# Kernel optimization log

Measured on AMD Instinct MI355X. Metric: run time of the kernel, lower is better.

Reference implementation:

```python
import jax, jax.numpy as jnp
import numpy as np

LN_EPS = 1e-5


def lstm_cell(x, h, c, Wih, Whh, b):
    # PyTorch gate order: i, f, g, o
    gates = x @ Wih.T + h @ Whh.T + b
    i, f, g, o = jnp.split(gates, 4, axis=-1)
    c = jax.nn.sigmoid(f) * c + jax.nn.sigmoid(i) * jnp.tanh(g)
    h = jax.nn.sigmoid(o) * jnp.tanh(c)
    return h, c


def run_lstm_layer(xs, Wih, Whh, b, reverse=False):
    # xs: (T, B, D) -> ys: (T, B, H); zero initial state, matching nn.LSTM default
    B = xs.shape[1]
    H = Whh.shape[1]
    init = (jnp.zeros((B, H), xs.dtype), jnp.zeros((B, H), xs.dtype))

    def step(carry, x):
        h, c = lstm_cell(x, carry[0], carry[1], Wih, Whh, b)
        return (h, c), h

    _, ys = jax.lax.scan(step, init, xs, reverse=reverse)
    return ys


def forward(x, enc0_Wih, enc0_Whh, enc0_b, enc1_Wih, enc1_Whh, enc1_b,
            fc_z_W, fc_z_b, ln_g, ln_b, fc_init_W, fc_init_b,
            dec0_Wih, dec0_Whh, dec0_b, dec1_Wih, dec1_Whh, dec1_b,
            fc_out_W, fc_out_b):
    B, T, In = x.shape
    H = dec0_Whh.shape[1]
    L = 2  # num_layers

    # ---------- Encoder: 2-layer bidirectional LSTM ----------
    xs = jnp.transpose(x, (1, 0, 2))  # (T, B, In)
    # layer 0 (index 0 = forward dir, 1 = backward dir)
    f0 = run_lstm_layer(xs, enc0_Wih[0], enc0_Whh[0], enc0_b[0], reverse=False)
    b0 = run_lstm_layer(xs, enc0_Wih[1], enc0_Whh[1], enc0_b[1], reverse=True)
    h0cat = jnp.concatenate([f0, b0], axis=-1)  # (T, B, 2H); inter-layer dropout = identity (eval)
    # layer 1
    f1 = run_lstm_layer(h0cat, enc1_Wih[0], enc1_Whh[0], enc1_b[0], reverse=False)
    b1 = run_lstm_layer(h0cat, enc1_Wih[1], enc1_Whh[1], enc1_b[1], reverse=True)
    last_out = jnp.concatenate([f1[-1], b1[-1]], axis=-1)  # (B, 2H) == out[:, -1, :]

    zz = last_out @ fc_z_W.T + fc_z_b  # dropout = identity in eval
    mu = jnp.mean(zz, axis=-1, keepdims=True)
    var = jnp.mean((zz - mu) ** 2, axis=-1, keepdims=True)
    z = (zz - mu) * jax.lax.rsqrt(var + LN_EPS) * ln_g + ln_b  # (B, latent)

    # torch: fc_init(z).view(num_layers, batch, hidden) -- raw row-major reshape
    h_init = (z @ fc_init_W.T + fc_init_b).reshape(L, B, H)
    c_init = jnp.zeros_like(h_init)

    inp0 = jnp.zeros((B, In), x.dtype)

    def dec_step(carry, _):
        inp, h0, c0, h1, c1 = carry
        h0, c0 = lstm_cell(inp, h0, c0, dec0_Wih, dec0_Whh, dec0_b)
        h1, c1 = lstm_cell(h0, h1, c1, dec1_Wih, dec1_Whh, dec1_b)
        pred = h1 @ fc_out_W.T + fc_out_b  # dropout = identity (eval)
        # teacher_forcing_ratio = 0.0 path: feed back detached prediction
        return (jax.lax.stop_gradient(pred), h0, c0, h1, c1), pred

    carry0 = (inp0, h_init[0], c_init[0], h_init[1], c_init[1])
    _, preds = jax.lax.scan(dec_step, carry0, None, length=T)  # (T, B, In)
    x_hat = jnp.transpose(preds, (1, 0, 2))  # (B, T, In)
    return x_hat, z


def setup_inputs() -> dict:
    key = jax.random.key(0)
    B, T, In, H, Lat = 2048, 100, 64, 128, 32
    ks = iter(jax.random.split(key, 32))
    s = 0.08  # weight scale for stability
    d = {
        'x': jax.random.normal(next(ks), (B, T, In), jnp.float32),
        'enc0_Wih': s * jax.random.normal(next(ks), (2, 4 * H, In), jnp.float32),
        'enc0_Whh': s * jax.random.normal(next(ks), (2, 4 * H, H), jnp.float32),
        'enc0_b': s * jax.random.normal(next(ks), (2, 4 * H), jnp.float32),
        'enc1_Wih': s * jax.random.normal(next(ks), (2, 4 * H, 2 * H), jnp.float32),
        'enc1_Whh': s * jax.random.normal(next(ks), (2, 4 * H, H), jnp.float32),
        'enc1_b': s * jax.random.normal(next(ks), (2, 4 * H), jnp.float32),
        'fc_z_W': s * jax.random.normal(next(ks), (Lat, 2 * H), jnp.float32),
        'fc_z_b': s * jax.random.normal(next(ks), (Lat,), jnp.float32),
        'ln_g': jnp.ones((Lat,), jnp.float32),
        'ln_b': jnp.zeros((Lat,), jnp.float32),
        'fc_init_W': s * jax.random.normal(next(ks), (2 * H, Lat), jnp.float32),
        'fc_init_b': s * jax.random.normal(next(ks), (2 * H,), jnp.float32),
        'dec0_Wih': s * jax.random.normal(next(ks), (4 * H, In), jnp.float32),
        'dec0_Whh': s * jax.random.normal(next(ks), (4 * H, H), jnp.float32),
        'dec0_b': s * jax.random.normal(next(ks), (4 * H,), jnp.float32),
        'dec1_Wih': s * jax.random.normal(next(ks), (4 * H, H), jnp.float32),
        'dec1_Whh': s * jax.random.normal(next(ks), (4 * H, H), jnp.float32),
        'dec1_b': s * jax.random.normal(next(ks), (4 * H,), jnp.float32),
        'fc_out_W': s * jax.random.normal(next(ks), (In, H), jnp.float32),
        'fc_out_b': s * jax.random.normal(next(ks), (In,), jnp.float32),
    }
    return d


def reference(x, enc0_Wih, enc0_Whh, enc0_b, enc1_Wih, enc1_Whh, enc1_b,
              fc_z_W, fc_z_b, ln_g, ln_b, fc_init_W, fc_init_b,
              dec0_Wih, dec0_Whh, dec0_b, dec1_Wih, dec1_Whh, dec1_b,
              fc_out_W, fc_out_b):
    return forward(x, enc0_Wih, enc0_Whh, enc0_b, enc1_Wih, enc1_Whh, enc1_b,
                   fc_z_W, fc_z_b, ln_g, ln_b, fc_init_W, fc_init_b,
                   dec0_Wih, dec0_Whh, dec0_b, dec1_Wih, dec1_Whh, dec1_b,
                   fc_out_W, fc_out_b)
```

## Files before the change

kernel.cpp:

```cpp
#include <hip/hip_runtime.h>

using u32 = unsigned int;
using u16 = unsigned short;

typedef __attribute__((ext_vector_type(8))) short bfrag;
typedef __attribute__((ext_vector_type(4))) float f32x4;

constexpr int T_ = 100, B_ = 2048;
constexpr size_t X_HAT_SZ = (size_t)B_ * T_ * 64;

constexpr size_t PKB    = 26214400;
constexpr size_t PK_A0  = PKB + 0;
constexpr size_t PK_A1  = PKB + 32768;
constexpr size_t PK_A2  = PKB + 65536;
constexpr size_t PK_A3  = PKB + 131072;
constexpr size_t PK_A4  = PKB + 196608;
constexpr size_t PK_A5  = PKB + 327680;
constexpr size_t PK_A6  = PKB + 458752;
constexpr size_t PK_A7  = PKB + 524288;
constexpr size_t PK_A8  = PKB + 557056;
constexpr size_t PK_A9  = PKB + 622592;
constexpr size_t PK_A10 = PKB + 688128;
constexpr size_t PK_A11 = PKB + 753664;
constexpr size_t PK_ENDU = PKB + 761856;
constexpr size_t O_FCZT  = PK_ENDU * 2;
constexpr size_t O_FCIT  = O_FCZT + 32768;
constexpr size_t O_FINIT = O_FCIT + 32768;

__device__ __forceinline__ u16 f2bfu(float f) {
  u32 u = __float_as_uint(f);
  u += 0x7fffu + ((u >> 16) & 1u);
  return (u16)(u >> 16);
}
__device__ __forceinline__ float bf2f(u32 s) { return __uint_as_float(s << 16); }

__device__ __forceinline__ float sigf(float v) {
  return __builtin_amdgcn_rcpf(1.f + __expf(-v));
}
__device__ __forceinline__ float tanhfast(float v) {
  float a = fabsf(v);
  float e = __expf(-2.f * a);
  float t = fmaf(-2.f * e, __builtin_amdgcn_rcpf(1.f + e), 1.f);
  return v < 0.f ? -t : t;
}

template <int N>
__device__ __forceinline__ void pinA(bfrag* W) {
#pragma unroll
  for (int i = 0; i < N; ++i) asm volatile("" : "+a"(W[i]));
}

__device__ __forceinline__ bfrag ldA(const u16* buf, int strideHalf, int kt, int lane) {
  return *(const bfrag*)(buf + (lane & 15) * strideHalf + kt * 32 + (lane >> 4) * 8);
}

template <int NKT>
__device__ __forceinline__ void mm(f32x4 acc[4], const bfrag* A, const u16* WP, int w, int lane) {
#pragma unroll
  for (int kt = 0; kt < NKT; ++kt) {
#pragma unroll
    for (int g = 0; g < 4; ++g) {
      bfrag bw = *(const bfrag*)(WP + (((size_t)(kt * 32 + g * 8 + w)) * 64 + lane) * 8);
      acc[g] = __builtin_amdgcn_mfma_f32_16x16x32_bf16(A[kt], bw, acc[g], 0, 0, 0);
    }
  }
}

template <int NKT>
__device__ __forceinline__ void loadW(bfrag* W, const u16* wsu, size_t base, int w, int lane) {
#pragma unroll
  for (int kt = 0; kt < NKT; ++kt)
#pragma unroll
    for (int g = 0; g < 4; ++g)
      W[kt * 4 + g] = *(const bfrag*)(wsu + base + (((size_t)(kt * 32 + g * 8 + w)) * 64 + lane) * 8);
}

template <int NKT>
__device__ __forceinline__ void mmR(f32x4 acc[4], const u16* lds, int sh, const bfrag* W, int lane) {
#pragma unroll
  for (int kt = 0; kt < NKT; ++kt) {
    bfrag a = ldA(lds, sh, kt, lane);
#pragma unroll
    for (int g = 0; g < 4; ++g)
      acc[g] = __builtin_amdgcn_mfma_f32_16x16x32_bf16(a, W[kt * 4 + g], acc[g], 0, 0, 0);
  }
}

template <int NKT>
__device__ __forceinline__ void mmL(f32x4 acc[4], const u16* alds, int sh,
                                    const u16* wlds, int w, int lane) {
#pragma unroll
  for (int kt = 0; kt < NKT; ++kt) {
    bfrag a = ldA(alds, sh, kt, lane);
#pragma unroll
    for (int g = 0; g < 4; ++g) {
      bfrag b = *(const bfrag*)(wlds + ((size_t)(kt * 32 + g * 8 + w) * 64 + lane) * 8);
      acc[g] = __builtin_amdgcn_mfma_f32_16x16x32_bf16(a, b, acc[g], 0, 0, 0);
    }
  }
}

__device__ __forceinline__ void cellfin(const f32x4 acc[4], float c[4], u16 hq[4]) {
#pragma unroll
  for (int q = 0; q < 4; ++q) {
    float iv = sigf(acc[0][q]);
    float fv = sigf(acc[1][q]);
    float gv = tanhfast(acc[2][q]);
    float ov = sigf(acc[3][q]);
    c[q] = fmaf(fv, c[q], iv * gv);
    hq[q] = f2bfu(ov * tanhfast(c[q]));
  }
}

__global__ void pack_kernel(const float* e0wih, const float* e0whh,
                            const float* e1wih, const float* e1whh,
                            const float* d0wih, const float* d0whh,
                            const float* d1wih, const float* d1whh,
                            const float* fczw, const float* fciw, const float* fcow,
                            char* ws) {
  int idx = blockIdx.x * 256 + threadIdx.x;
  u16* wsu = (u16*)ws;

  const float* srcs[12] = { e0wih, e0wih + 512 * 64, e0whh, e0whh + 512 * 128,
                            e1wih, e1wih + 512 * 256, e1whh,
                            d0wih, d0whh, d1wih, d1whh, fcow };
  const int Ks[12]  = { 64, 64, 128, 128, 256, 256, 128, 64, 128, 128, 128, 128 };
  const int NFs[12] = { 32, 32, 32, 32, 32, 32, 32, 32, 32, 32, 32, 4 };
  const int cnt[12] = { 32768, 32768, 65536, 65536, 131072, 131072, 65536,
                        32768, 65536, 65536, 65536, 8192 };
  const size_t dst[12] = { PK_A0, PK_A1, PK_A2, PK_A3, PK_A4, PK_A5, PK_A6,
                           PK_A7, PK_A8, PK_A9, PK_A10, PK_A11 };
#pragma unroll
  for (int p = 0; p < 12; ++p) {
    if (idx < cnt[p]) {
      int NF = NFs[p], K = Ks[p];
      int kt = idx / (NF * 512);
      int rem = idx - kt * NF * 512;
      int nf = rem >> 9;
      int li = rem & 511;
      int lane = li >> 3, j = li & 7;
      int n = nf * 16 + (lane & 15);
      int k = kt * 32 + (lane >> 4) * 8 + j;
      wsu[dst[p] + idx] = f2bfu(srcs[p][(size_t)n * K + k]);
      return;
    }
    idx -= cnt[p];
  }
  if (idx < 8192) {
    int k = idx >> 5, l = idx & 31;
    ((float*)(ws + O_FCZT))[idx] = fczw[(size_t)l * 256 + k];
    return;
  }
  idx -= 8192;
  if (idx < 8192) {
    int l = idx >> 8, o = idx & 255;
    ((float*)(ws + O_FCIT))[idx] = fciw[(size_t)o * 32 + l];
    return;
  }
}
constexpr int PACK_TOTAL = 761856 + 16384;
constexpr int PACK_GRID = (PACK_TOTAL + 255) / 256;

__global__ __attribute__((amdgpu_flat_work_group_size(512, 512), amdgpu_waves_per_eu(2, 2)))
void enc01_kernel(
    const float* __restrict__ x, const float* __restrict__ e0b,
    char* __restrict__ ws, float* __restrict__ out) {
  __shared__ __align__(16) u16 xbuf[2][16 * 72];
  __shared__ __align__(16) u16 hbuf[2][16 * 136];

  const int tid = threadIdx.x;
  const int lane = tid & 63, w = tid >> 6;
  const int mode = blockIdx.x >> 7;
  const int chunk = blockIdx.x & 127;
  const int b0r = chunk * 16;
  const u16* wsu = (const u16*)ws;
  const int uu = 16 * w + (lane & 15);
  const int rg = lane >> 4;
  const bool rev = (mode == 0);
  u16* dst = rev ? (u16*)out : (u16*)ws;

  bfrag Wi[8], Wh[16];
  loadW<2>(Wi, wsu, rev ? PK_A1 : PK_A0, w, lane);
  loadW<4>(Wh, wsu, rev ? PK_A3 : PK_A2, w, lane);
  pinA<8>(Wi);
  pinA<16>(Wh);
  const float* bias = e0b + (rev ? 512 : 0);
  const float bi = bias[uu], bf = bias[128 + uu], bg = bias[256 + uu], bo = bias[384 + uu];

  const int xr = tid >> 5, xcp = (tid & 31) * 2;
  auto ldx = [&](int t) {
    return *(const float2*)(x + ((size_t)(b0r + xr) * T_ + t) * 64 + xcp);
  };

  for (int i = tid; i < 2 * 16 * 136; i += 512) (&hbuf[0][0])[i] = 0;
  float c[4] = {0.f, 0.f, 0.f, 0.f};
  float2 pf = ldx(rev ? T_ - 1 : 0);
  *(u32*)&xbuf[0][xr * 72 + xcp] = ((u32)f2bfu(pf.y) << 16) | f2bfu(pf.x);
  __syncthreads();
  pf = ldx(rev ? T_ - 2 : 1);

  int p = 0;
  for (int s = 0; s < T_; ++s) {
    int t = rev ? T_ - 1 - s : s;
    f32x4 acc[4] = { {bi,bi,bi,bi}, {bf,bf,bf,bf}, {bg,bg,bg,bg}, {bo,bo,bo,bo} };
    mmR<2>(acc, xbuf[p], 72, Wi, lane);
    mmR<4>(acc, hbuf[p], 136, Wh, lane);
    u16 hq[4];
    cellfin(acc, c, hq);
#pragma unroll
    for (int q = 0; q < 4; ++q) {
      int row = rg * 4 + q;
      hbuf[1 - p][row * 136 + uu] = hq[q];
      dst[(((size_t)chunk * T_ + t) * 16 + row) * 128 + uu] = hq[q];
    }
    if (s < T_ - 1)
      *(u32*)&xbuf[1 - p][xr * 72 + xcp] = ((u32)f2bfu(pf.y) << 16) | f2bfu(pf.x);
    if (s < T_ - 2) pf = ldx(rev ? t - 2 : t + 2);
    __syncthreads();
    p ^= 1;
  }
}

constexpr int E2_A6   = 0;
constexpr int E2_CAT  = 131072;
constexpr int E2_HB   = 147968;
constexpr int E2_LAST = 0;
constexpr int E2_ZB   = 16384;

__global__ __attribute__((amdgpu_flat_work_group_size(512, 512), amdgpu_waves_per_eu(2, 2)))
void enc2_kernel(
    const float* __restrict__ e1b, const float* __restrict__ fczb,
    const float* __restrict__ lng, const float* __restrict__ lnb,
    const float* __restrict__ fcib,
    char* __restrict__ ws, float* __restrict__ out) {
  __shared__ __align__(16) char sm[156672];
  u16* A6L = (u16*)(sm + E2_A6);

  const int tid = threadIdx.x;
  const int lane = tid & 63, w = tid >> 6;
  const int chunk = blockIdx.x;
  const int b0r = chunk * 16;
  const u16* wsu = (const u16*)ws;
  const int uu = 16 * w + (lane & 15);
  const int rg = lane >> 4;

  {
    const uint4* src = (const uint4*)(wsu + PK_A6);
    uint4* d = (uint4*)A6L;
    for (int i = tid; i < 8192; i += 512) d[i] = src[i];
  }
  bfrag W4[32];
  loadW<8>(W4, wsu, PK_A4, w, lane);
  pinA<32>(W4);
  const float bi = e1b[uu], bf = e1b[128 + uu], bg = e1b[256 + uu], bo = e1b[384 + uu];
  {
    u16* hb0 = (u16*)(sm + E2_HB);
    for (int i = tid; i < 2 * 16 * 136; i += 512) hb0[i] = 0;
  }
  float c[4] = {0.f, 0.f, 0.f, 0.f};

  const u32* f0u = (const u32*)ws;
  const u32* b0u = (const u32*)out;
  const int prow = tid >> 6, pc4 = tid & 63;
  auto ldrow = [&](const u32* src, int t, int r) {
    return src[(((size_t)chunk * T_ + t) * 16 + r) * 64 + pc4];
  };
  u32 pa = ldrow(f0u, 0, prow), pb = ldrow(f0u, 0, prow + 8);
  u32 pc = ldrow(b0u, 0, prow), pd = ldrow(b0u, 0, prow + 8);
  {
    u16* cat0 = (u16*)(sm + E2_CAT);
    *(u32*)&cat0[prow * 264 + pc4 * 2] = pa;
    *(u32*)&cat0[(prow + 8) * 264 + pc4 * 2] = pb;
    *(u32*)&cat0[prow * 264 + 128 + pc4 * 2] = pc;
    *(u32*)&cat0[(prow + 8) * 264 + 128 + pc4 * 2] = pd;
  }
  __syncthreads();
  pa = ldrow(f0u, 1, prow); pb = ldrow(f0u, 1, prow + 8);
  pc = ldrow(b0u, 1, prow); pd = ldrow(b0u, 1, prow + 8);

  int p = 0;
  for (int t = 0; t < T_; ++t) {
    u16* catP = (u16*)(sm + E2_CAT + p * 8448);
    u16* catN = (u16*)(sm + E2_CAT + (1 - p) * 8448);
    u16* hbP  = (u16*)(sm + E2_HB + p * 4352);
    u16* hbN  = (u16*)(sm + E2_HB + (1 - p) * 4352);
    f32x4 acc[4] = { {bi,bi,bi,bi}, {bf,bf,bf,bf}, {bg,bg,bg,bg}, {bo,bo,bo,bo} };
    mmR<8>(acc, catP, 264, W4, lane);
    mmL<4>(acc, hbP, 136, A6L, w, lane);
    if (t < T_ - 1) {
      *(u32*)&catN[prow * 264 + pc4 * 2] = pa;
      *(u32*)&catN[(prow + 8) * 264 + pc4 * 2] = pb;
      *(u32*)&catN[prow * 264 + 128 + pc4 * 2] = pc;
      *(u32*)&catN[(prow + 8) * 264 + 128 + pc4 * 2] = pd;
    }
    if (t < T_ - 2) {
      pa = ldrow(f0u, t + 2, prow); pb = ldrow(f0u, t + 2, prow + 8);
      pc = ldrow(b0u, t + 2, prow); pd = ldrow(b0u, t + 2, prow + 8);
    }
    u16 hq[4];
    cellfin(acc, c, hq);
#pragma unroll
    for (int q = 0; q < 4; ++q) hbN[(rg * 4 + q) * 136 + uu] = hq[q];
    __syncthreads();
    p ^= 1;
  }

  float* lastout = (float*)(sm + E2_LAST);
  float* zbuf = (float*)(sm + E2_ZB);
  {
    u16* cat99 = (u16*)(sm + E2_CAT + 8448);
    u16* hb99  = (u16*)(sm + E2_HB);
    const float* b = e1b + 512;
    float bi2 = b[uu], bf2 = b[128 + uu], bg2 = b[256 + uu], bo2 = b[384 + uu];
    bfrag a8[8];
#pragma unroll
    for (int kt = 0; kt < 8; ++kt) a8[kt] = ldA(cat99, 264, kt, lane);
    f32x4 acc[4] = { {bi2,bi2,bi2,bi2}, {bf2,bf2,bf2,bf2}, {bg2,bg2,bg2,bg2}, {bo2,bo2,bo2,bo2} };
    mm<8>(acc, a8, wsu + PK_A5, w, lane);
    __syncthreads();
#pragma unroll
    for (int q = 0; q < 4; ++q) {
      float iv = sigf(acc[0][q]);
      float gv = tanhfast(acc[2][q]);
      float ov = sigf(acc[3][q]);
      float cv = iv * gv;
      lastout[(rg * 4 + q) * 256 + 128 + uu] = ov * tanhfast(cv);
    }
    for (int i = tid; i < 2048; i += 512) {
      int r = i >> 7, cc = i & 127;
      lastout[r * 256 + cc] = bf2f(hb99[r * 136 + cc]);
    }
    __syncthreads();
  }

  {
    int r = tid >> 5, l = tid & 31;
    const float* fczT = (const float*)(ws + O_FCZT);
    float acc = fczb[l];
    for (int k = 0; k < 256; ++k) acc = fmaf(lastout[r * 256 + k], fczT[k * 32 + l], acc);
    float s1 = acc, s2 = acc * acc;
#pragma unroll
    for (int off = 16; off >= 1; off >>= 1) {
      s1 += __shfl_xor(s1, off, 32);
      s2 += __shfl_xor(s2, off, 32);
    }
    float mu = s1 * (1.f / 32.f);
    float var = s2 * (1.f / 32.f) - mu * mu;
    float zv = (acc - mu) * rsqrtf(var + 1e-5f) * lng[l] + lnb[l];
    zbuf[r * 32 + l] = zv;
    out[X_HAT_SZ + (size_t)(b0r + r) * 32 + l] = zv;
  }
  __syncthreads();

  {
    const float* fciT = (const float*)(ws + O_FCIT);
    float* finit = (float*)(ws + O_FINIT);
    int o = tid & 255, half = tid >> 8;
#pragma unroll
    for (int rr = 0; rr < 8; ++rr) {
      int r = half * 8 + rr;
      float acc = fcib[o];
#pragma unroll
      for (int l = 0; l < 32; ++l) acc = fmaf(zbuf[r * 32 + l], fciT[l * 256 + o], acc);
      finit[(size_t)(b0r + r) * 256 + o] = acc;
    }
  }
}

constexpr int DC_A10 = 0;
constexpr int DC_XB  = 131072;
constexpr int DC_HA  = 135680;
constexpr int DC_HB  = 144384;
__global__ __attribute__((amdgpu_flat_work_group_size(512, 512), amdgpu_waves_per_eu(2, 2)))
void dec_kernel(
    const float* __restrict__ d0b, const float* __restrict__ d1b,
    const float* __restrict__ fcob,
    char* __restrict__ ws, float* __restrict__ out) {
  __shared__ __align__(16) char sm[153088];
  u16* A10L = (u16*)(sm + DC_A10);

  const int tid = threadIdx.x;
  const int lane = tid & 63, w = tid >> 6;
  const int chunk = blockIdx.x;
  const int b0r = chunk * 16;
  const u16* wsu = (const u16*)ws;
  const float* finit = (const float*)(ws + O_FINIT);
  const int uu = 16 * w + (lane & 15);
  const int rg = lane >> 4;

  {
    const uint4* src = (const uint4*)(wsu + PK_A10);
    uint4* d = (uint4*)A10L;
    for (int i = tid; i < 8192; i += 512) d[i] = src[i];
  }
  bfrag W7[8], W8[16], W9[16], W11[4];
  loadW<2>(W7, wsu, PK_A7, w, lane);
  loadW<4>(W8, wsu, PK_A8, w, lane);
  loadW<4>(W9, wsu, PK_A9, w, lane);
  {
    int wf = w & 3;
#pragma unroll
    for (int kt = 0; kt < 4; ++kt)
      W11[kt] = *(const bfrag*)(wsu + PK_A11 + (((size_t)(kt * 4 + wf)) * 64 + lane) * 8);
  }
  pinA<8>(W7);
  pinA<16>(W8);
  pinA<16>(W9);
  pinA<4>(W11);

  {
    u16* xb0 = (u16*)(sm + DC_XB);
    for (int i = tid; i < 2 * 16 * 72; i += 512) xb0[i] = 0;
    u16* ha0 = (u16*)(sm + DC_HA);
    u16* hb0 = (u16*)(sm + DC_HB);
    for (int i = tid; i < 2048; i += 512) {
      int r = i >> 7, j = i & 127;
      int b = b0r + r;
      ha0[r * 136 + j] = f2bfu(finit[(size_t)(b >> 1) * 256 + (b & 1) * 128 + j]);
      hb0[r * 136 + j] = f2bfu(finit[(size_t)(1024 + (b >> 1)) * 256 + (b & 1) * 128 + j]);
    }
  }
  const float d0i = d0b[uu], d0f = d0b[128 + uu], d0g = d0b[256 + uu], d0o = d0b[384 + uu];
  const float d1i = d1b[uu], d1f = d1b[128 + uu], d1g = d1b[256 + uu], d1o = d1b[384 + uu];
  const float fob = (w < 4) ? fcob[16 * w + (lane & 15)] : 0.f;
  float c0[4] = {0.f, 0.f, 0.f, 0.f}, c1[4] = {0.f, 0.f, 0.f, 0.f};
  __syncthreads();

  int p = 0;
  for (int t = 0; t < T_; ++t) {
    u16* xbP = (u16*)(sm + DC_XB + p * 2304);
    u16* xbN = (u16*)(sm + DC_XB + (1 - p) * 2304);
    u16* haP = (u16*)(sm + DC_HA + p * 4352);
    u16* haN = (u16*)(sm + DC_HA + (1 - p) * 4352);
    u16* hbP = (u16*)(sm + DC_HB + p * 4352);
    u16* hbN = (u16*)(sm + DC_HB + (1 - p) * 4352);
    {
      f32x4 acc[4] = { {d0i,d0i,d0i,d0i}, {d0f,d0f,d0f,d0f}, {d0g,d0g,d0g,d0g}, {d0o,d0o,d0o,d0o} };
      mmR<2>(acc, xbP, 72, W7, lane);
      mmR<4>(acc, haP, 136, W8, lane);
      u16 hq[4];
      cellfin(acc, c0, hq);
#pragma unroll
      for (int q = 0; q < 4; ++q) haN[(rg * 4 + q) * 136 + uu] = hq[q];
    }
    __syncthreads();
    {
      f32x4 acc[4] = { {d1i,d1i,d1i,d1i}, {d1f,d1f,d1f,d1f}, {d1g,d1g,d1g,d1g}, {d1o,d1o,d1o,d1o} };
      mmR<4>(acc, haN, 136, W9, lane);
      mmL<4>(acc, hbP, 136, A10L, w, lane);
      u16 hq[4];
      cellfin(acc, c1, hq);
#pragma unroll
      for (int q = 0; q < 4; ++q) hbN[(rg * 4 + q) * 136 + uu] = hq[q];
    }
    __syncthreads();
    if (w < 4) {
      f32x4 accP = {fob, fob, fob, fob};
#pragma unroll
      for (int kt = 0; kt < 4; ++kt) {
        bfrag a = ldA(hbN, 136, kt, lane);
        accP = __builtin_amdgcn_mfma_f32_16x16x32_bf16(a, W11[kt], accP, 0, 0, 0);
      }
      int oc = 16 * w + (lane & 15);
#pragma unroll
      for (int q = 0; q < 4; ++q) {
        int row = rg * 4 + q;
        float pv = accP[q];
        out[((size_t)(b0r + row) * T_ + t) * 64 + oc] = pv;
        xbN[row * 72 + oc] = f2bfu(pv);
      }
    }
    __syncthreads();
    p ^= 1;
  }
}

extern "C" void kernel_launch(void* const* d_in, const int* in_sizes, int n_in,
                              void* d_out, int out_size, void* d_ws, size_t ws_size,
                              hipStream_t stream) {
  const float* x     = (const float*)d_in[0];
  const float* e0wih = (const float*)d_in[1];
  const float* e0whh = (const float*)d_in[2];
  const float* e0b   = (const float*)d_in[3];
  const float* e1wih = (const float*)d_in[4];
  const float* e1whh = (const float*)d_in[5];
  const float* e1b   = (const float*)d_in[6];
  const float* fczw  = (const float*)d_in[7];
  const float* fczb  = (const float*)d_in[8];
  const float* lng   = (const float*)d_in[9];
  const float* lnb   = (const float*)d_in[10];
  const float* fciw  = (const float*)d_in[11];
  const float* fcib  = (const float*)d_in[12];
  const float* d0wih = (const float*)d_in[13];
  const float* d0whh = (const float*)d_in[14];
  const float* d0b   = (const float*)d_in[15];
  const float* d1wih = (const float*)d_in[16];
  const float* d1whh = (const float*)d_in[17];
  const float* d1b   = (const float*)d_in[18];
  const float* fcow  = (const float*)d_in[19];
  const float* fcob  = (const float*)d_in[20];
  char* ws = (char*)d_ws;
  float* out = (float*)d_out;

  pack_kernel<<<PACK_GRID, 256, 0, stream>>>(e0wih, e0whh, e1wih, e1whh,
                                             d0wih, d0whh, d1wih, d1whh,
                                             fczw, fciw, fcow, ws);
  enc01_kernel<<<256, 512, 0, stream>>>(x, e0b, ws, out);
  enc2_kernel<<<128, 512, 0, stream>>>(e1b, fczb, lng, lnb, fcib, ws, out);
  dec_kernel<<<128, 512, 0, stream>>>(d0b, d1b, fcob, ws, out);
}
```

Before: 622.9 us.

## Halve LSTM block size to 4 waves, each computing two hidden-unit groups

Every recurrent kernel now launches 256 threads instead of 512. Each wave owns two 16-unit column groups and keeps twice as many weight fragments resident in AGPRs (waves_per_eu 1). The per-step MFMA A-fragment loads from LDS are shared across both groups, and fewer waves take part in each barrier. Global loads and LDS stores are widened to match. In exchange, per-wave latency rises and register pressure is very high, with up to 64 pinned fragments plus doubled accumulators.

```diff
diff --git a/kernel.cpp b/kernel.cpp
--- a/kernel.cpp
+++ b/kernel.cpp
@@ -55,48 +55,60 @@
 }
 
 template <int NKT>
-__device__ __forceinline__ void mm(f32x4 acc[4], const bfrag* A, const u16* WP, int w, int lane) {
-#pragma unroll
-  for (int kt = 0; kt < NKT; ++kt) {
-#pragma unroll
-    for (int g = 0; g < 4; ++g) {
-      bfrag bw = *(const bfrag*)(WP + (((size_t)(kt * 32 + g * 8 + w)) * 64 + lane) * 8);
-      acc[g] = __builtin_amdgcn_mfma_f32_16x16x32_bf16(A[kt], bw, acc[g], 0, 0, 0);
-    }
+__device__ __forceinline__ void loadW2(bfrag W[2][NKT * 4], const u16* wsu, size_t base,
+                                       int w, int lane) {
+#pragma unroll
+  for (int u2 = 0; u2 < 2; ++u2) {
+    int ug = w + u2 * 4;
+#pragma unroll
+    for (int kt = 0; kt < NKT; ++kt)
+#pragma unroll
+      for (int g = 0; g < 4; ++g)
+        W[u2][kt * 4 + g] =
+            *(const bfrag*)(wsu + base + (((size_t)(kt * 32 + g * 8 + ug)) * 64 + lane) * 8);
   }
 }
 
 template <int NKT>
-__device__ __forceinline__ void loadW(bfrag* W, const u16* wsu, size_t base, int w, int lane) {
-#pragma unroll
-  for (int kt = 0; kt < NKT; ++kt)
-#pragma unroll
-    for (int g = 0; g < 4; ++g)
-      W[kt * 4 + g] = *(const bfrag*)(wsu + base + (((size_t)(kt * 32 + g * 8 + w)) * 64 + lane) * 8);
-}
-
-template <int NKT>
-__device__ __forceinline__ void mmR(f32x4 acc[4], const u16* lds, int sh, const bfrag* W, int lane) {
+__device__ __forceinline__ void mm2(f32x4 acc[2][4], const u16* lds, int sh,
+                                    const bfrag W[2][NKT * 4], int lane) {
 #pragma unroll
   for (int kt = 0; kt < NKT; ++kt) {
     bfrag a = ldA(lds, sh, kt, lane);
 #pragma unroll
-    for (int g = 0; g < 4; ++g)
-      acc[g] = __builtin_amdgcn_mfma_f32_16x16x32_bf16(a, W[kt * 4 + g], acc[g], 0, 0, 0);
+    for (int u2 = 0; u2 < 2; ++u2)
+#pragma unroll
+      for (int g = 0; g < 4; ++g)
+        acc[u2][g] = __builtin_amdgcn_mfma_f32_16x16x32_bf16(a, W[u2][kt * 4 + g], acc[u2][g], 0, 0, 0);
   }
 }
 
 template <int NKT>
-__device__ __forceinline__ void mmL(f32x4 acc[4], const u16* alds, int sh,
-                                    const u16* wlds, int w, int lane) {
+__device__ __forceinline__ void mm2L(f32x4 acc[2][4], const u16* alds, int sh,
+                                     const u16* wlds, int w, int lane) {
 #pragma unroll
   for (int kt = 0; kt < NKT; ++kt) {
     bfrag a = ldA(alds, sh, kt, lane);
 #pragma unroll
-    for (int g = 0; g < 4; ++g) {
-      bfrag b = *(const bfrag*)(wlds + ((size_t)(kt * 32 + g * 8 + w) * 64 + lane) * 8);
-      acc[g] = __builtin_amdgcn_mfma_f32_16x16x32_bf16(a, b, acc[g], 0, 0, 0);
-    }
+    for (int u2 = 0; u2 < 2; ++u2) {
+      int ug = w + u2 * 4;
+#pragma unroll
+      for (int g = 0; g < 4; ++g) {
+        bfrag b = *(const bfrag*)(wlds + ((size_t)(kt * 32 + g * 8 + ug) * 64 + lane) * 8);
+        acc[u2][g] = __builtin_amdgcn_mfma_f32_16x16x32_bf16(a, b, acc[u2][g], 0, 0, 0);
+      }
+    }
+  }
+}
+
+__device__ __forceinline__ void accInit(f32x4 acc[2][4], const float* bI, const float* bF,
+                                        const float* bG, const float* bO) {
+#pragma unroll
+  for (int u2 = 0; u2 < 2; ++u2) {
+    acc[u2][0] = {bI[u2], bI[u2], bI[u2], bI[u2]};
+    acc[u2][1] = {bF[u2], bF[u2], bF[u2], bF[u2]};
+    acc[u2][2] = {bG[u2], bG[u2], bG[u2], bG[u2]};
+    acc[u2][3] = {bO[u2], bO[u2], bO[u2], bO[u2]};
   }
 }
 
@@ -161,7 +173,7 @@
 constexpr int PACK_TOTAL = 761856 + 16384;
 constexpr int PACK_GRID = (PACK_TOTAL + 255) / 256;
 
-__global__ __attribute__((amdgpu_flat_work_group_size(512, 512), amdgpu_waves_per_eu(2, 2)))
+__global__ __attribute__((amdgpu_flat_work_group_size(256, 256), amdgpu_waves_per_eu(1, 1)))
 void enc01_kernel(
     const float* __restrict__ x, const float* __restrict__ e0b,
     char* __restrict__ ws, float* __restrict__ out) {
@@ -174,47 +186,57 @@
   const int chunk = blockIdx.x & 127;
   const int b0r = chunk * 16;
   const u16* wsu = (const u16*)ws;
-  const int uu = 16 * w + (lane & 15);
   const int rg = lane >> 4;
   const bool rev = (mode == 0);
   u16* dst = rev ? (u16*)out : (u16*)ws;
-
-  bfrag Wi[8], Wh[16];
-  loadW<2>(Wi, wsu, rev ? PK_A1 : PK_A0, w, lane);
-  loadW<4>(Wh, wsu, rev ? PK_A3 : PK_A2, w, lane);
-  pinA<8>(Wi);
-  pinA<16>(Wh);
+  const int uuA = 16 * w + (lane & 15), uuB = uuA + 64;
+
+  bfrag Wi[2][8], Wh[2][16];
+  loadW2<2>(Wi, wsu, rev ? PK_A1 : PK_A0, w, lane);
+  loadW2<4>(Wh, wsu, rev ? PK_A3 : PK_A2, w, lane);
+  pinA<16>(&Wi[0][0]);
+  pinA<32>(&Wh[0][0]);
   const float* bias = e0b + (rev ? 512 : 0);
-  const float bi = bias[uu], bf = bias[128 + uu], bg = bias[256 + uu], bo = bias[384 + uu];
-
-  const int xr = tid >> 5, xcp = (tid & 31) * 2;
+  float bI[2] = {bias[uuA], bias[uuB]}, bF[2] = {bias[128 + uuA], bias[128 + uuB]},
+        bG[2] = {bias[256 + uuA], bias[256 + uuB]}, bO[2] = {bias[384 + uuA], bias[384 + uuB]};
+
+  const int xr = tid >> 4, xcp = (tid & 15) * 4;
   auto ldx = [&](int t) {
-    return *(const float2*)(x + ((size_t)(b0r + xr) * T_ + t) * 64 + xcp);
+    return *(const float4*)(x + ((size_t)(b0r + xr) * T_ + t) * 64 + xcp);
   };
-
-  for (int i = tid; i < 2 * 16 * 136; i += 512) (&hbuf[0][0])[i] = 0;
-  float c[4] = {0.f, 0.f, 0.f, 0.f};
-  float2 pf = ldx(rev ? T_ - 1 : 0);
-  *(u32*)&xbuf[0][xr * 72 + xcp] = ((u32)f2bfu(pf.y) << 16) | f2bfu(pf.x);
+  auto stx = [&](int pb, float4 v) {
+    u32 lo = ((u32)f2bfu(v.y) << 16) | f2bfu(v.x);
+    u32 hi = ((u32)f2bfu(v.w) << 16) | f2bfu(v.z);
+    *(uint2*)&xbuf[pb][xr * 72 + xcp] = make_uint2(lo, hi);
+  };
+
+  for (int i = tid; i < 2 * 16 * 136; i += 256) (&hbuf[0][0])[i] = 0;
+  float c[2][4] = {};
+  float4 pf = ldx(rev ? T_ - 1 : 0);
+  stx(0, pf);
   __syncthreads();
   pf = ldx(rev ? T_ - 2 : 1);
 
   int p = 0;
   for (int s = 0; s < T_; ++s) {
     int t = rev ? T_ - 1 - s : s;
-    f32x4 acc[4] = { {bi,bi,bi,bi}, {bf,bf,bf,bf}, {bg,bg,bg,bg}, {bo,bo,bo,bo} };
-    mmR<2>(acc, xbuf[p], 72, Wi, lane);
-    mmR<4>(acc, hbuf[p], 136, Wh, lane);
-    u16 hq[4];
-    cellfin(acc, c, hq);
-#pragma unroll
-    for (int q = 0; q < 4; ++q) {
-      int row = rg * 4 + q;
-      hbuf[1 - p][row * 136 + uu] = hq[q];
-      dst[(((size_t)chunk * T_ + t) * 16 + row) * 128 + uu] = hq[q];
-    }
-    if (s < T_ - 1)
-      *(u32*)&xbuf[1 - p][xr * 72 + xcp] = ((u32)f2bfu(pf.y) << 16) | f2bfu(pf.x);
+    f32x4 acc[2][4];
+    accInit(acc, bI, bF, bG, bO);
+    mm2<2>(acc, xbuf[p], 72, Wi, lane);
+    mm2<4>(acc, hbuf[p], 136, Wh, lane);
+#pragma unroll
+    for (int u2 = 0; u2 < 2; ++u2) {
+      u16 hq[4];
+      cellfin(acc[u2], c[u2], hq);
+      int uu2 = u2 ? uuB : uuA;
+#pragma unroll
+      for (int q = 0; q < 4; ++q) {
+        int row = rg * 4 + q;
+        hbuf[1 - p][row * 136 + uu2] = hq[q];
+        dst[(((size_t)chunk * T_ + t) * 16 + row) * 128 + uu2] = hq[q];
+      }
+    }
+    if (s < T_ - 1) stx(1 - p, pf);
     if (s < T_ - 2) pf = ldx(rev ? t - 2 : t + 2);
     __syncthreads();
     p ^= 1;
@@ -227,7 +249,7 @@
 constexpr int E2_LAST = 0;
 constexpr int E2_ZB   = 16384;
 
-__global__ __attribute__((amdgpu_flat_work_group_size(512, 512), amdgpu_waves_per_eu(2, 2)))
+__global__ __attribute__((amdgpu_flat_work_group_size(256, 256), amdgpu_waves_per_eu(1, 1)))
 void enc2_kernel(
     const float* __restrict__ e1b, const float* __restrict__ fczb,
     const float* __restrict__ lng, const float* __restrict__ lnb,
@@ -241,42 +263,43 @@
   const int chunk = blockIdx.x;
   const int b0r = chunk * 16;
   const u16* wsu = (const u16*)ws;
-  const int uu = 16 * w + (lane & 15);
   const int rg = lane >> 4;
+  const int uuA = 16 * w + (lane & 15), uuB = uuA + 64;
 
   {
     const uint4* src = (const uint4*)(wsu + PK_A6);
     uint4* d = (uint4*)A6L;
-    for (int i = tid; i < 8192; i += 512) d[i] = src[i];
-  }
-  bfrag W4[32];
-  loadW<8>(W4, wsu, PK_A4, w, lane);
-  pinA<32>(W4);
-  const float bi = e1b[uu], bf = e1b[128 + uu], bg = e1b[256 + uu], bo = e1b[384 + uu];
+    for (int i = tid; i < 8192; i += 256) d[i] = src[i];
+  }
+  bfrag W4[2][32];
+  loadW2<8>(W4, wsu, PK_A4, w, lane);
+  pinA<64>(&W4[0][0]);
+  float bI[2] = {e1b[uuA], e1b[uuB]}, bF[2] = {e1b[128 + uuA], e1b[128 + uuB]},
+        bG[2] = {e1b[256 + uuA], e1b[256 + uuB]}, bO[2] = {e1b[384 + uuA], e1b[384 + uuB]};
   {
     u16* hb0 = (u16*)(sm + E2_HB);
-    for (int i = tid; i < 2 * 16 * 136; i += 512) hb0[i] = 0;
-  }
-  float c[4] = {0.f, 0.f, 0.f, 0.f};
-
-  const u32* f0u = (const u32*)ws;
-  const u32* b0u = (const u32*)out;
-  const int prow = tid >> 6, pc4 = tid & 63;
-  auto ldrow = [&](const u32* src, int t, int r) {
-    return src[(((size_t)chunk * T_ + t) * 16 + r) * 64 + pc4];
+    for (int i = tid; i < 2 * 16 * 136; i += 256) hb0[i] = 0;
+  }
+  float c[2][4] = {};
+
+  const uint2* f0v = (const uint2*)ws;
+  const uint2* b0v = (const uint2*)out;
+  const int prow = tid >> 5, pc2 = tid & 31;
+  auto ldrow = [&](const uint2* src, int t, int r) {
+    return src[(((size_t)chunk * T_ + t) * 16 + r) * 32 + pc2];
   };
-  u32 pa = ldrow(f0u, 0, prow), pb = ldrow(f0u, 0, prow + 8);
-  u32 pc = ldrow(b0u, 0, prow), pd = ldrow(b0u, 0, prow + 8);
+  uint2 pa = ldrow(f0v, 0, prow), pb = ldrow(f0v, 0, prow + 8);
+  uint2 pc = ldrow(b0v, 0, prow), pd = ldrow(b0v, 0, prow + 8);
   {
     u16* cat0 = (u16*)(sm + E2_CAT);
-    *(u32*)&cat0[prow * 264 + pc4 * 2] = pa;
-    *(u32*)&cat0[(prow + 8) * 264 + pc4 * 2] = pb;
-    *(u32*)&cat0[prow * 264 + 128 + pc4 * 2] = pc;
-    *(u32*)&cat0[(prow + 8) * 264 + 128 + pc4 * 2] = pd;
+    *(uint2*)&cat0[prow * 264 + pc2 * 4] = pa;
+    *(uint2*)&cat0[(prow + 8) * 264 + pc2 * 4] = pb;
+    *(uint2*)&cat0[prow * 264 + 128 + pc2 * 4] = pc;
+    *(uint2*)&cat0[(prow + 8) * 264 + 128 + pc2 * 4] = pd;
   }
   __syncthreads();
-  pa = ldrow(f0u, 1, prow); pb = ldrow(f0u, 1, prow + 8);
-  pc = ldrow(b0u, 1, prow); pd = ldrow(b0u, 1, prow + 8);
+  pa = ldrow(f0v, 1, prow); pb = ldrow(f0v, 1, prow + 8);
+  pc = ldrow(b0v, 1, prow); pd = ldrow(b0v, 1, prow + 8);
 
   int p = 0;
   for (int t = 0; t < T_; ++t) {
@@ -284,23 +307,28 @@
     u16* catN = (u16*)(sm + E2_CAT + (1 - p) * 8448);
     u16* hbP  = (u16*)(sm + E2_HB + p * 4352);
     u16* hbN  = (u16*)(sm + E2_HB + (1 - p) * 4352);
-    f32x4 acc[4] = { {bi,bi,bi,bi}, {bf,bf,bf,bf}, {bg,bg,bg,bg}, {bo,bo,bo,bo} };
-    mmR<8>(acc, catP, 264, W4, lane);
-    mmL<4>(acc, hbP, 136, A6L, w, lane);
+    f32x4 acc[2][4];
+    accInit(acc, bI, bF, bG, bO);
+    mm2<8>(acc, catP, 264, W4, lane);
+    mm2L<4>(acc, hbP, 136, A6L, w, lane);
     if (t < T_ - 1) {
-      *(u32*)&catN[prow * 264 + pc4 * 2] = pa;
-      *(u32*)&catN[(prow + 8) * 264 + pc4 * 2] = pb;
-      *(u32*)&catN[prow * 264 + 128 + pc4 * 2] = pc;
-      *(u32*)&catN[(prow + 8) * 264 + 128 + pc4 * 2] = pd;
+      *(uint2*)&catN[prow * 264 + pc2 * 4] = pa;
+      *(uint2*)&catN[(prow + 8) * 264 + pc2 * 4] = pb;
+      *(uint2*)&catN[prow * 264 + 128 + pc2 * 4] = pc;
+      *(uint2*)&catN[(prow + 8) * 264 + 128 + pc2 * 4] = pd;
     }
     if (t < T_ - 2) {
-      pa = ldrow(f0u, t + 2, prow); pb = ldrow(f0u, t + 2, prow + 8);
-      pc = ldrow(b0u, t + 2, prow); pd = ldrow(b0u, t + 2, prow + 8);
-    }
-    u16 hq[4];
-    cellfin(acc, c, hq);
-#pragma unroll
-    for (int q = 0; q < 4; ++q) hbN[(rg * 4 + q) * 136 + uu] = hq[q];
+      pa = ldrow(f0v, t + 2, prow); pb = ldrow(f0v, t + 2, prow + 8);
+      pc = ldrow(b0v, t + 2, prow); pd = ldrow(b0v, t + 2, prow + 8);
+    }
+#pragma unroll
+    for (int u2 = 0; u2 < 2; ++u2) {
+      u16 hq[4];
+      cellfin(acc[u2], c[u2], hq);
+      int uu2 = u2 ? uuB : uuA;
+#pragma unroll
+      for (int q = 0; q < 4; ++q) hbN[(rg * 4 + q) * 136 + uu2] = hq[q];
+    }
     __syncthreads();
     p ^= 1;
   }
@@ -311,22 +339,38 @@
     u16* cat99 = (u16*)(sm + E2_CAT + 8448);
     u16* hb99  = (u16*)(sm + E2_HB);
     const float* b = e1b + 512;
-    float bi2 = b[uu], bf2 = b[128 + uu], bg2 = b[256 + uu], bo2 = b[384 + uu];
+    float cI[2] = {b[uuA], b[uuB]}, cF[2] = {b[128 + uuA], b[128 + uuB]},
+          cG[2] = {b[256 + uuA], b[256 + uuB]}, cO[2] = {b[384 + uuA], b[384 + uuB]};
     bfrag a8[8];
 #pragma unroll
     for (int kt = 0; kt < 8; ++kt) a8[kt] = ldA(cat99, 264, kt, lane);
-    f32x4 acc[4] = { {bi2,bi2,bi2,bi2}, {bf2,bf2,bf2,bf2}, {bg2,bg2,bg2,bg2}, {bo2,bo2,bo2,bo2} };
-    mm<8>(acc, a8, wsu + PK_A5, w, lane);
-    __syncthreads();
-#pragma unroll
-    for (int q = 0; q < 4; ++q) {
-      float iv = sigf(acc[0][q]);
-      float gv = tanhfast(acc[2][q]);
-      float ov = sigf(acc[3][q]);
-      float cv = iv * gv;
-      lastout[(rg * 4 + q) * 256 + 128 + uu] = ov * tanhfast(cv);
-    }
-    for (int i = tid; i < 2048; i += 512) {
+    f32x4 acc[2][4];
+    accInit(acc, cI, cF, cG, cO);
+#pragma unroll
+    for (int kt = 0; kt < 8; ++kt)
+#pragma unroll
+      for (int u2 = 0; u2 < 2; ++u2) {
+        int ug = w + u2 * 4;
+#pragma unroll
+        for (int g = 0; g < 4; ++g) {
+          bfrag bw = *(const bfrag*)(wsu + PK_A5 +
+              (((size_t)(kt * 32 + g * 8 + ug)) * 64 + lane) * 8);
+          acc[u2][g] = __builtin_amdgcn_mfma_f32_16x16x32_bf16(a8[kt], bw, acc[u2][g], 0, 0, 0);
+        }
+      }
+#pragma unroll
+    for (int u2 = 0; u2 < 2; ++u2) {
+      int uu2 = u2 ? uuB : uuA;
+#pragma unroll
+      for (int q = 0; q < 4; ++q) {
+        float iv = sigf(acc[u2][0][q]);
+        float gv = tanhfast(acc[u2][2][q]);
+        float ov = sigf(acc[u2][3][q]);
+        float cv = iv * gv;
+        lastout[(rg * 4 + q) * 256 + 128 + uu2] = ov * tanhfast(cv);
+      }
+    }
+    for (int i = tid; i < 2048; i += 256) {
       int r = i >> 7, cc = i & 127;
       lastout[r * 256 + cc] = bf2f(hb99[r * 136 + cc]);
     }
@@ -334,31 +378,34 @@
   }
 
   {
-    int r = tid >> 5, l = tid & 31;
+    int r0 = tid >> 5, l = tid & 31;
     const float* fczT = (const float*)(ws + O_FCZT);
-    float acc = fczb[l];
-    for (int k = 0; k < 256; ++k) acc = fmaf(lastout[r * 256 + k], fczT[k * 32 + l], acc);
-    float s1 = acc, s2 = acc * acc;
-#pragma unroll
-    for (int off = 16; off >= 1; off >>= 1) {
-      s1 += __shfl_xor(s1, off, 32);
-      s2 += __shfl_xor(s2, off, 32);
-    }
-    float mu = s1 * (1.f / 32.f);
-    float var = s2 * (1.f / 32.f) - mu * mu;
-    float zv = (acc - mu) * rsqrtf(var + 1e-5f) * lng[l] + lnb[l];
-    zbuf[r * 32 + l] = zv;
-    out[X_HAT_SZ + (size_t)(b0r + r) * 32 + l] = zv;
+#pragma unroll
+    for (int half = 0; half < 2; ++half) {
+      int r = r0 + half * 8;
+      float acc = fczb[l];
+      for (int k = 0; k < 256; ++k) acc = fmaf(lastout[r * 256 + k], fczT[k * 32 + l], acc);
+      float s1 = acc, s2 = acc * acc;
+#pragma unroll
+      for (int off = 16; off >= 1; off >>= 1) {
+        s1 += __shfl_xor(s1, off, 32);
+        s2 += __shfl_xor(s2, off, 32);
+      }
+      float mu = s1 * (1.f / 32.f);
+      float var = s2 * (1.f / 32.f) - mu * mu;
+      float zv = (acc - mu) * rsqrtf(var + 1e-5f) * lng[l] + lnb[l];
+      zbuf[r * 32 + l] = zv;
+      out[X_HAT_SZ + (size_t)(b0r + r) * 32 + l] = zv;
+    }
   }
   __syncthreads();
 
   {
     const float* fciT = (const float*)(ws + O_FCIT);
     float* finit = (float*)(ws + O_FINIT);
-    int o = tid & 255, half = tid >> 8;
-#pragma unroll
-    for (int rr = 0; rr < 8; ++rr) {
-      int r = half * 8 + rr;
+    int o = tid;
+#pragma unroll
+    for (int r = 0; r < 16; ++r) {
       float acc = fcib[o];
 #pragma unroll
       for (int l = 0; l < 32; ++l) acc = fmaf(zbuf[r * 32 + l], fciT[l * 256 + o], acc);
@@ -371,7 +418,7 @@
 constexpr int DC_XB  = 131072;
 constexpr int DC_HA  = 135680;
 constexpr int DC_HB  = 144384;
-__global__ __attribute__((amdgpu_flat_work_group_size(512, 512), amdgpu_waves_per_eu(2, 2)))
+__global__ __attribute__((amdgpu_flat_work_group_size(256, 256), amdgpu_waves_per_eu(1, 1)))
 void dec_kernel(
     const float* __restrict__ d0b, const float* __restrict__ d1b,
     const float* __restrict__ fcob,
@@ -385,45 +432,42 @@
   const int b0r = chunk * 16;
   const u16* wsu = (const u16*)ws;
   const float* finit = (const float*)(ws + O_FINIT);
-  const int uu = 16 * w + (lane & 15);
   const int rg = lane >> 4;
+  const int uuA = 16 * w + (lane & 15), uuB = uuA + 64;
 
   {
     const uint4* src = (const uint4*)(wsu + PK_A10);
     uint4* d = (uint4*)A10L;
-    for (int i = tid; i < 8192; i += 512) d[i] = src[i];
-  }
-  bfrag W7[8], W8[16], W9[16], W11[4];
-  loadW<2>(W7, wsu, PK_A7, w, lane);
-  loadW<4>(W8, wsu, PK_A8, w, lane);
-  loadW<4>(W9, wsu, PK_A9, w, lane);
-  {
-    int wf = w & 3;
-#pragma unroll
-    for (int kt = 0; kt < 4; ++kt)
-      W11[kt] = *(const bfrag*)(wsu + PK_A11 + (((size_t)(kt * 4 + wf)) * 64 + lane) * 8);
-  }
-  pinA<8>(W7);
-  pinA<16>(W8);
-  pinA<16>(W9);
-  pinA<4>(W11);
+    for (int i = tid; i < 8192; i += 256) d[i] = src[i];
+  }
+  bfrag W7[2][8], W8[2][16], W9[2][16], W11[4];
+  loadW2<2>(W7, wsu, PK_A7, w, lane);
+  loadW2<4>(W8, wsu, PK_A8, w, lane);
+  loadW2<4>(W9, wsu, PK_A9, w, lane);
+#pragma unroll
+  for (int kt = 0; kt < 4; ++kt)
+    W11[kt] = *(const bfrag*)(wsu + PK_A11 + (((size_t)(kt * 4 + w)) * 64 + lane) * 8);
+  pinA<32>(&W8[0][0]);
+  pinA<32>(&W9[0][0]);
 
   {
     u16* xb0 = (u16*)(sm + DC_XB);
-    for (int i = tid; i < 2 * 16 * 72; i += 512) xb0[i] = 0;
+    for (int i = tid; i < 2 * 16 * 72; i += 256) xb0[i] = 0;
     u16* ha0 = (u16*)(sm + DC_HA);
     u16* hb0 = (u16*)(sm + DC_HB);
-    for (int i = tid; i < 2048; i += 512) {
+    for (int i = tid; i < 2048; i += 256) {
       int r = i >> 7, j = i & 127;
       int b = b0r + r;
       ha0[r * 136 + j] = f2bfu(finit[(size_t)(b >> 1) * 256 + (b & 1) * 128 + j]);
       hb0[r * 136 + j] = f2bfu(finit[(size_t)(1024 + (b >> 1)) * 256 + (b & 1) * 128 + j]);
     }
   }
-  const float d0i = d0b[uu], d0f = d0b[128 + uu], d0g = d0b[256 + uu], d0o = d0b[384 + uu];
-  const float d1i = d1b[uu], d1f = d1b[128 + uu], d1g = d1b[256 + uu], d1o = d1b[384 + uu];
-  const float fob = (w < 4) ? fcob[16 * w + (lane & 15)] : 0.f;
-  float c0[4] = {0.f, 0.f, 0.f, 0.f}, c1[4] = {0.f, 0.f, 0.f, 0.f};
+  float aI[2] = {d0b[uuA], d0b[uuB]}, aF[2] = {d0b[128 + uuA], d0b[128 + uuB]},
+        aG[2] = {d0b[256 + uuA], d0b[256 + uuB]}, aO[2] = {d0b[384 + uuA], d0b[384 + uuB]};
+  float eI[2] = {d1b[uuA], d1b[uuB]}, eF[2] = {d1b[128 + uuA], d1b[128 + uuB]},
+        eG[2] = {d1b[256 + uuA], d1b[256 + uuB]}, eO[2] = {d1b[384 + uuA], d1b[384 + uuB]};
+  const float fob = fcob[16 * w + (lane & 15)];
+  float c0[2][4] = {}, c1[2][4] = {};
   __syncthreads();
 
   int p = 0;
@@ -435,26 +479,36 @@
     u16* hbP = (u16*)(sm + DC_HB + p * 4352);
     u16* hbN = (u16*)(sm + DC_HB + (1 - p) * 4352);
     {
-      f32x4 acc[4] = { {d0i,d0i,d0i,d0i}, {d0f,d0f,d0f,d0f}, {d0g,d0g,d0g,d0g}, {d0o,d0o,d0o,d0o} };
-      mmR<2>(acc, xbP, 72, W7, lane);
-      mmR<4>(acc, haP, 136, W8, lane);
-      u16 hq[4];
-      cellfin(acc, c0, hq);
-#pragma unroll
-      for (int q = 0; q < 4; ++q) haN[(rg * 4 + q) * 136 + uu] = hq[q];
+      f32x4 acc[2][4];
+      accInit(acc, aI, aF, aG, aO);
+      mm2<2>(acc, xbP, 72, W7, lane);
+      mm2<4>(acc, haP, 136, W8, lane);
+#pragma unroll
+      for (int u2 = 0; u2 < 2; ++u2) {
+        u16 hq[4];
+        cellfin(acc[u2], c0[u2], hq);
+        int uu2 = u2 ? uuB : uuA;
+#pragma unroll
+        for (int q = 0; q < 4; ++q) haN[(rg * 4 + q) * 136 + uu2] = hq[q];
+      }
     }
     __syncthreads();
     {
-      f32x4 acc[4] = { {d1i,d1i,d1i,d1i}, {d1f,d1f,d1f,d1f}, {d1g,d1g,d1g,d1g}, {d1o,d1o,d1o,d1o} };
-      mmR<4>(acc, haN, 136, W9, lane);
-      mmL<4>(acc, hbP, 136, A10L, w, lane);
-      u16 hq[4];
-      cellfin(acc, c1, hq);
-#pragma unroll
-      for (int q = 0; q < 4; ++q) hbN[(rg * 4 + q) * 136 + uu] = hq[q];
+      f32x4 acc[2][4];
+      accInit(acc, eI, eF, eG, eO);
+      mm2<4>(acc, haN, 136, W9, lane);
+      mm2L<4>(acc, hbP, 136, A10L, w, lane);
+#pragma unroll
+      for (int u2 = 0; u2 < 2; ++u2) {
+        u16 hq[4];
+        cellfin(acc[u2], c1[u2], hq);
+        int uu2 = u2 ? uuB : uuA;
+#pragma unroll
+        for (int q = 0; q < 4; ++q) hbN[(rg * 4 + q) * 136 + uu2] = hq[q];
+      }
     }
     __syncthreads();
-    if (w < 4) {
+    {
       f32x4 accP = {fob, fob, fob, fob};
 #pragma unroll
       for (int kt = 0; kt < 4; ++kt) {
@@ -505,7 +559,7 @@
   pack_kernel<<<PACK_GRID, 256, 0, stream>>>(e0wih, e0whh, e1wih, e1whh,
                                              d0wih, d0whh, d1wih, d1whh,
                                              fczw, fciw, fcow, ws);
-  enc01_kernel<<<256, 512, 0, stream>>>(x, e0b, ws, out);
-  enc2_kernel<<<128, 512, 0, stream>>>(e1b, fczb, lng, lnb, fcib, ws, out);
-  dec_kernel<<<128, 512, 0, stream>>>(d0b, d1b, fcob, ws, out);
-}
+  enc01_kernel<<<256, 256, 0, stream>>>(x, e0b, ws, out);
+  enc2_kernel<<<128, 256, 0, stream>>>(e1b, fczb, lng, lnb, fcib, ws, out);
+  dec_kernel<<<128, 256, 0, stream>>>(d0b, d1b, fcob, ws, out);
+}
```

New measurement: 774.5 us. +24.3%, slower.
